# Performance work log

Hardware: AMD Instinct MI355X
Metric: run time of the kernel (lower is better)

Reference implementation:

```python
import jax, jax.numpy as jnp
import numpy as np

N = 100000
E = 1600000
IN_DIM, HID, NCLS = 256, 128, 40


def setup_inputs() -> dict:
    key = jax.random.key(0)
    ks = jax.random.split(key, 8)
    x = jax.random.normal(ks[0], (N, IN_DIM), dtype=jnp.float32)
    edge_index = jax.random.randint(ks[1], (2, E), 0, N, dtype=jnp.int32)
    def glorot(k, shape):
        lim = float(np.sqrt(6.0 / (shape[0] + shape[1])))
        return jax.random.uniform(k, shape, jnp.float32, -lim, lim)
    return {
        "x": x,
        "edge_index": edge_index,
        "W1": glorot(ks[2], (IN_DIM, HID)), "b1": jnp.zeros((HID,), jnp.float32),
        "W2": glorot(ks[3], (HID, HID)),    "b2": jnp.zeros((HID,), jnp.float32),
        "W3": glorot(ks[4], (HID, NCLS)),   "b3": jnp.zeros((NCLS,), jnp.float32),
    }


def _gcn_conv(x, src, dst, W, b):
    # dense transform first (PyG GCNConv applies lin before propagate)
    h = x @ W  # [N, out]
    # symmetric normalization with self-loops: deg over destination (in-degree)
    ones = jnp.ones(src.shape[0], dtype=x.dtype)
    deg = jax.ops.segment_sum(ones, dst, num_segments=N)
    dinv = jnp.where(deg > 0, jax.lax.rsqrt(jnp.maximum(deg, 1e-12)), 0.0)
    norm = dinv[src] * dinv[dst]  # [E+N]
    msgs = h[src] * norm[:, None]  # gather + scale
    out = jax.ops.segment_sum(msgs, dst, num_segments=N)
    return out + b


def reference(x, edge_index, W1, b1, W2, b2, W3, b3):
    # add self-loops once (same for every layer)
    loop = jnp.arange(N, dtype=edge_index.dtype)
    src = jnp.concatenate([edge_index[0], loop])
    dst = jnp.concatenate([edge_index[1], loop])
    h = _gcn_conv(x, src, dst, W1, b1)
    h = jax.nn.relu(h)  # dropout is identity in eval mode
    h = _gcn_conv(h, src, dst, W2, b2)
    h = jax.nn.relu(h)
    h = _gcn_conv(h, src, dst, W3, b3)
    return h
```

## Files before the change

### kernel.cpp

```cpp
#include <hip/hip_runtime.h>
#include <hip/hip_bf16.h>


#define WAVE 64
#define SLOTS 48
#define FILL_NR 8
#define FILL_NCHUNK 784

typedef short short8v __attribute__((ext_vector_type(8)));
typedef float f32x4 __attribute__((ext_vector_type(4)));

__device__ inline void split_bf16(float v, ushort& hi, ushort& lo) {
    __hip_bfloat16 h = __float2bfloat16(v);
    float hf = __bfloat162float(h);
    __hip_bfloat16 l = __float2bfloat16(v - hf);
    hi = *reinterpret_cast<ushort*>(&h);
    lo = *reinterpret_cast<ushort*>(&l);
}

__device__ inline float bf2f(ushort u) {
    unsigned int t = ((unsigned int)u) << 16;
    return __uint_as_float(t);
}

__device__ inline float bfLo(unsigned int u) { return __uint_as_float(u << 16); }
__device__ inline float bfHi(unsigned int u) { return __uint_as_float(u & 0xffff0000u); }

__device__ inline ushort f2bf(float v) {
    __hip_bfloat16 h = __float2bfloat16(v);
    return *reinterpret_cast<ushort*>(&h);
}


__global__ void k_fill_part(const int* __restrict__ src, const int* __restrict__ dst,
                            int* __restrict__ cnt, int* __restrict__ slots,
                            int E, int N) {
    int b = blockIdx.x;
    int r = b & (FILL_NR - 1);
    int c = b >> 3;
    int lo = (int)((long long)E * c / FILL_NCHUNK);
    int hi = (int)((long long)E * (c + 1) / FILL_NCHUNK);
    int rlo = (int)((long long)N * r / FILL_NR);
    int rhi = (int)((long long)N * (r + 1) / FILL_NR);
    for (int e = lo + threadIdx.x; e < hi; e += 256) {
        int d = dst[e];
        if (d >= rlo && d < rhi) {
            int p = atomicAdd(&cnt[d], 1);
            if (p < SLOTS) slots[(size_t)d * SLOTS + p] = src[e];
        }
    }
}

__global__ void k_dinv(const int* __restrict__ cnt, float* __restrict__ dinv, int N) {
    int i = blockIdx.x * blockDim.x + threadIdx.x;
    if (i < N) dinv[i] = rsqrtf((float)cnt[i] + 1.0f);
}


__global__ void k_wsplit(const float* __restrict__ W, ushort* __restrict__ Wth,
                         ushort* __restrict__ Wtl, int K, int M, int Mpad) {
    int idx = blockIdx.x * 256 + threadIdx.x;
    if (idx >= K * Mpad) return;
    int k = idx / Mpad, m = idx % Mpad;
    float v = (m < M) ? W[(size_t)k * M + m] : 0.f;
    ushort h, l;
    split_bf16(v, h, l);
    Wth[(size_t)m * K + k] = h;
    Wtl[(size_t)m * K + k] = l;
}


template <int K, bool BF16OUT>
__global__ __launch_bounds__(256) void gemm_mfma128(const float* __restrict__ A,
                                                    const ushort* __restrict__ Wth,
                                                    const ushort* __restrict__ Wtl,
                                                    const float* __restrict__ rowscale,
                                                    void* __restrict__ outv, int N) {
    constexpr int KC = 32;
    constexpr int LD = 40;
    __shared__ ushort Ah[128 * LD], Al[128 * LD], Bh[128 * LD], Bl[128 * LD];

    const int tid = threadIdx.x;
    const int lane = tid & 63, wave = tid >> 6;
    const int wr = (wave & 1) * 64, wc = (wave >> 1) * 64;
    const int r0 = blockIdx.x * 128;
    const int tr = lane & 15, quad = lane >> 4;

    f32x4 acc[4][4];
#pragma unroll
    for (int i = 0; i < 4; ++i)
#pragma unroll
        for (int j = 0; j < 4; ++j) acc[i][j] = (f32x4)(0.f);

    float4 pa[4];
    uint4 pbh[2], pbl[2];
    auto loadc = [&](int kc) {
#pragma unroll
        for (int u = 0; u < 4; ++u) {
            int f = tid + u * 256;
            int row = f >> 3, kq = f & 7;
            int grow = r0 + row;
            if (grow > N - 1) grow = N - 1;
            pa[u] = *reinterpret_cast<const float4*>(A + (size_t)grow * K + kc + kq * 4);
        }
#pragma unroll
        for (int u = 0; u < 2; ++u) {
            int f = tid + u * 256;
            int col = f >> 2, part = f & 3;
            pbh[u] = *reinterpret_cast<const uint4*>(Wth + (size_t)col * K + kc + part * 8);
            pbl[u] = *reinterpret_cast<const uint4*>(Wtl + (size_t)col * K + kc + part * 8);
        }
    };

    loadc(0);
    for (int kc = 0; kc < K; kc += KC) {
#pragma unroll
        for (int u = 0; u < 4; ++u) {
            int f = tid + u * 256;
            int row = f >> 3, kq = f & 7;
            float4 v = pa[u];
            ushort h0, l0, h1, l1, h2, l2, h3, l3;
            split_bf16(v.x, h0, l0);
            split_bf16(v.y, h1, l1);
            split_bf16(v.z, h2, l2);
            split_bf16(v.w, h3, l3);
            *reinterpret_cast<ushort4*>(&Ah[row * LD + kq * 4]) = make_ushort4(h0, h1, h2, h3);
            *reinterpret_cast<ushort4*>(&Al[row * LD + kq * 4]) = make_ushort4(l0, l1, l2, l3);
        }
#pragma unroll
        for (int u = 0; u < 2; ++u) {
            int f = tid + u * 256;
            int col = f >> 2, part = f & 3;
            *reinterpret_cast<uint4*>(&Bh[col * LD + part * 8]) = pbh[u];
            *reinterpret_cast<uint4*>(&Bl[col * LD + part * 8]) = pbl[u];
        }
        __syncthreads();
        if (kc + KC < K) loadc(kc + KC);
        short8v ah[4], al[4], bh[4], bl[4];
#pragma unroll
        for (int i = 0; i < 4; ++i) {
            ah[i] = *reinterpret_cast<const short8v*>(&Ah[(wr + i * 16 + tr) * LD + quad * 8]);
            al[i] = *reinterpret_cast<const short8v*>(&Al[(wr + i * 16 + tr) * LD + quad * 8]);
            bh[i] = *reinterpret_cast<const short8v*>(&Bh[(wc + i * 16 + tr) * LD + quad * 8]);
            bl[i] = *reinterpret_cast<const short8v*>(&Bl[(wc + i * 16 + tr) * LD + quad * 8]);
        }
#pragma unroll
        for (int i = 0; i < 4; ++i)
#pragma unroll
            for (int j = 0; j < 4; ++j) {
                acc[i][j] = __builtin_amdgcn_mfma_f32_16x16x32_bf16(ah[i], bh[j], acc[i][j], 0, 0, 0);
                acc[i][j] = __builtin_amdgcn_mfma_f32_16x16x32_bf16(ah[i], bl[j], acc[i][j], 0, 0, 0);
                acc[i][j] = __builtin_amdgcn_mfma_f32_16x16x32_bf16(al[i], bh[j], acc[i][j], 0, 0, 0);
            }
        __syncthreads();
    }

#pragma unroll
    for (int i = 0; i < 4; ++i) {
        int rbase = r0 + wr + i * 16 + quad * 4;
        float rs[4];
#pragma unroll
        for (int reg = 0; reg < 4; ++reg) {
            int r = rbase + reg;
            rs[reg] = (r < N) ? rowscale[r] : 0.f;
        }
#pragma unroll
        for (int j = 0; j < 4; ++j) {
            int c = wc + j * 16 + tr;
#pragma unroll
            for (int reg = 0; reg < 4; ++reg) {
                int r = rbase + reg;
                if (r < N) {
                    float v = acc[i][j][reg] * rs[reg];
                    if (BF16OUT)
                        ((ushort*)outv)[(size_t)r * 128 + c] = f2bf(v);
                    else
                        ((float*)outv)[(size_t)r * 128 + c] = v;
                }
            }
        }
    }
}


__global__ __launch_bounds__(256) void gemm_mfma40(const float* __restrict__ A,
                                                   const ushort* __restrict__ Wth,
                                                   const ushort* __restrict__ Wtl,
                                                   const float* __restrict__ rowscale,
                                                   float* __restrict__ out, int N) {
    constexpr int K = 128, KC = 32, LD = 40, M = 40;
    __shared__ ushort Ah[128 * LD], Al[128 * LD], Bh[48 * LD], Bl[48 * LD];

    const int tid = threadIdx.x;
    const int lane = tid & 63, wave = tid >> 6;
    const int wr = wave * 32;
    const int r0 = blockIdx.x * 128;
    const int tr = lane & 15, quad = lane >> 4;
    const bool hasb = tid < 192;

    f32x4 acc[2][3];
#pragma unroll
    for (int i = 0; i < 2; ++i)
#pragma unroll
        for (int j = 0; j < 3; ++j) acc[i][j] = (f32x4)(0.f);

    float4 pa[4];
    uint4 pbh0, pbl0;
    auto loadc = [&](int kc) {
#pragma unroll
        for (int u = 0; u < 4; ++u) {
            int f = tid + u * 256;
            int row = f >> 3, kq = f & 7;
            int grow = r0 + row;
            if (grow > N - 1) grow = N - 1;
            pa[u] = *reinterpret_cast<const float4*>(A + (size_t)grow * K + kc + kq * 4);
        }
        if (hasb) {
            int col = tid >> 2, part = tid & 3;
            pbh0 = *reinterpret_cast<const uint4*>(Wth + (size_t)col * K + kc + part * 8);
            pbl0 = *reinterpret_cast<const uint4*>(Wtl + (size_t)col * K + kc + part * 8);
        }
    };

    loadc(0);
    for (int kc = 0; kc < K; kc += KC) {
#pragma unroll
        for (int u = 0; u < 4; ++u) {
            int f = tid + u * 256;
            int row = f >> 3, kq = f & 7;
            float4 v = pa[u];
            ushort h0, l0, h1, l1, h2, l2, h3, l3;
            split_bf16(v.x, h0, l0);
            split_bf16(v.y, h1, l1);
            split_bf16(v.z, h2, l2);
            split_bf16(v.w, h3, l3);
            *reinterpret_cast<ushort4*>(&Ah[row * LD + kq * 4]) = make_ushort4(h0, h1, h2, h3);
            *reinterpret_cast<ushort4*>(&Al[row * LD + kq * 4]) = make_ushort4(l0, l1, l2, l3);
        }
        if (hasb) {
            int col = tid >> 2, part = tid & 3;
            *reinterpret_cast<uint4*>(&Bh[col * LD + part * 8]) = pbh0;
            *reinterpret_cast<uint4*>(&Bl[col * LD + part * 8]) = pbl0;
        }
        __syncthreads();
        if (kc + KC < K) loadc(kc + KC);
        short8v ah[2], al[2], bh[3], bl[3];
#pragma unroll
        for (int i = 0; i < 2; ++i) {
            ah[i] = *reinterpret_cast<const short8v*>(&Ah[(wr + i * 16 + tr) * LD + quad * 8]);
            al[i] = *reinterpret_cast<const short8v*>(&Al[(wr + i * 16 + tr) * LD + quad * 8]);
        }
#pragma unroll
        for (int j = 0; j < 3; ++j) {
            bh[j] = *reinterpret_cast<const short8v*>(&Bh[(j * 16 + tr) * LD + quad * 8]);
            bl[j] = *reinterpret_cast<const short8v*>(&Bl[(j * 16 + tr) * LD + quad * 8]);
        }
#pragma unroll
        for (int i = 0; i < 2; ++i)
#pragma unroll
            for (int j = 0; j < 3; ++j) {
                acc[i][j] = __builtin_amdgcn_mfma_f32_16x16x32_bf16(ah[i], bh[j], acc[i][j], 0, 0, 0);
                acc[i][j] = __builtin_amdgcn_mfma_f32_16x16x32_bf16(ah[i], bl[j], acc[i][j], 0, 0, 0);
                acc[i][j] = __builtin_amdgcn_mfma_f32_16x16x32_bf16(al[i], bh[j], acc[i][j], 0, 0, 0);
            }
        __syncthreads();
    }

#pragma unroll
    for (int i = 0; i < 2; ++i) {
        int rbase = r0 + wr + i * 16 + quad * 4;
        float rs[4];
#pragma unroll
        for (int reg = 0; reg < 4; ++reg) {
            int r = rbase + reg;
            rs[reg] = (r < N) ? rowscale[r] : 0.f;
        }
#pragma unroll
        for (int j = 0; j < 3; ++j) {
            int c = j * 16 + tr;
#pragma unroll
            for (int reg = 0; reg < 4; ++reg) {
                int r = rbase + reg;
                if (r < N && c < M) out[(size_t)r * M + c] = acc[i][j][reg] * rs[reg];
            }
        }
    }
}


template <bool RELU>
__global__ __launch_bounds__(256) void agg128_bf4(const ushort* __restrict__ S,
                                                  const int* __restrict__ slots,
                                                  const int* __restrict__ cnt,
                                                  const float* __restrict__ dinv,
                                                  const float* __restrict__ bias,
                                                  float* __restrict__ out, int N) {
    int w = (blockIdx.x * blockDim.x + threadIdx.x) >> 6;
    int lane = threadIdx.x & 63;
    int nquad = (N + 3) >> 2;
    if (w >= nquad) return;
    int part = lane >> 4, sub = lane & 15;
    int node = 4 * w + part;
    bool valid = node < N;
    int snode = valid ? node : 0;
    const uint4* S8 = (const uint4*)S;
    const int* row = slots + (size_t)snode * SLOTS;
    int c = valid ? cnt[snode] : 0;
    if (c > SLOTS) c = SLOTS;
    int cm = max(c, __shfl(c, lane ^ 16));
    cm = max(cm, __shfl(cm, lane ^ 32));

    uint4 sv = S8[(size_t)snode * 16 + sub];
    float a0 = bfLo(sv.x), a1 = bfHi(sv.x), a2 = bfLo(sv.y), a3 = bfHi(sv.y);
    float a4 = bfLo(sv.z), a5 = bfHi(sv.z), a6 = bfLo(sv.w), a7 = bfHi(sv.w);

    int e = 0;
    for (; e + 8 <= cm; e += 8) {
        int s[8];
#pragma unroll
        for (int u = 0; u < 8; ++u) s[u] = (e + u < c) ? row[e + u] : snode;
        uint4 v[8];
#pragma unroll
        for (int u = 0; u < 8; ++u) v[u] = S8[(size_t)s[u] * 16 + sub];
#pragma unroll
        for (int u = 0; u < 8; ++u) {
            float m = (e + u < c) ? 1.f : 0.f;
            a0 += m * bfLo(v[u].x);
            a1 += m * bfHi(v[u].x);
            a2 += m * bfLo(v[u].y);
            a3 += m * bfHi(v[u].y);
            a4 += m * bfLo(v[u].z);
            a5 += m * bfHi(v[u].z);
            a6 += m * bfLo(v[u].w);
            a7 += m * bfHi(v[u].w);
        }
    }
    for (; e < cm; ++e) {
        int s = (e < c) ? row[e] : snode;
        uint4 v = S8[(size_t)s * 16 + sub];
        float m = (e < c) ? 1.f : 0.f;
        a0 += m * bfLo(v.x);
        a1 += m * bfHi(v.x);
        a2 += m * bfLo(v.y);
        a3 += m * bfHi(v.y);
        a4 += m * bfLo(v.z);
        a5 += m * bfHi(v.z);
        a6 += m * bfLo(v.w);
        a7 += m * bfHi(v.w);
    }

    if (valid) {
        float di = dinv[node];
        float4 b0 = ((const float4*)bias)[sub * 2];
        float4 b1 = ((const float4*)bias)[sub * 2 + 1];
        float o0 = a0 * di + b0.x, o1 = a1 * di + b0.y, o2 = a2 * di + b0.z, o3 = a3 * di + b0.w;
        float o4 = a4 * di + b1.x, o5 = a5 * di + b1.y, o6 = a6 * di + b1.z, o7 = a7 * di + b1.w;
        if (RELU) {
            o0 = fmaxf(o0, 0.f); o1 = fmaxf(o1, 0.f); o2 = fmaxf(o2, 0.f); o3 = fmaxf(o3, 0.f);
            o4 = fmaxf(o4, 0.f); o5 = fmaxf(o5, 0.f); o6 = fmaxf(o6, 0.f); o7 = fmaxf(o7, 0.f);
        }
        ((float4*)out)[(size_t)node * 32 + sub * 2] = make_float4(o0, o1, o2, o3);
        ((float4*)out)[(size_t)node * 32 + sub * 2 + 1] = make_float4(o4, o5, o6, o7);
    }
}

__global__ __launch_bounds__(256) void agg40(const float* __restrict__ S,
                                             const int* __restrict__ slots,
                                             const int* __restrict__ cnt,
                                             const float* __restrict__ dinv,
                                             const float* __restrict__ bias,
                                             float* __restrict__ out, int N) {
    int wid = (blockIdx.x * blockDim.x + threadIdx.x) >> 6;
    int lane = threadIdx.x & 63;
    if (wid >= N || lane >= 40) return;
    const int* row = slots + (size_t)wid * SLOTS;
    int c = cnt[wid];
    if (c > SLOTS) c = SLOTS;
    float acc = S[(size_t)wid * 40 + lane];
    int e = 0;
    for (; e + 8 <= c; e += 8) {
        int s[8];
#pragma unroll
        for (int u = 0; u < 8; ++u) s[u] = row[e + u];
        float v[8];
#pragma unroll
        for (int u = 0; u < 8; ++u) v[u] = S[(size_t)s[u] * 40 + lane];
#pragma unroll
        for (int u = 0; u < 8; ++u) acc += v[u];
    }
    for (; e < c; ++e) acc += S[(size_t)row[e] * 40 + lane];
    out[(size_t)wid * 40 + lane] = acc * dinv[wid] + bias[lane];
}


extern "C" void kernel_launch(void* const* d_in, const int* in_sizes, int n_in,
                              void* d_out, int out_size, void* d_ws, size_t ws_size,
                              hipStream_t stream) {
    const float* x  = (const float*)d_in[0];
    const int*   ei = (const int*)d_in[1];
    const float* W1 = (const float*)d_in[2];
    const float* b1 = (const float*)d_in[3];
    const float* W2 = (const float*)d_in[4];
    const float* b2 = (const float*)d_in[5];
    const float* W3 = (const float*)d_in[6];
    const float* b3 = (const float*)d_in[7];
    float* out = (float*)d_out;

    const int IN_DIM = 256, HID = 128;
    const int N = in_sizes[0] / IN_DIM;
    const int E = in_sizes[1] / 2;
    const int* srcE = ei;
    const int* dstE = ei + E;

    char* ws = (char*)d_ws;
    size_t off = 0;
    auto alloc = [&](size_t bytes) -> void* {
        off = (off + 255) & ~(size_t)255;
        void* p = ws + off;
        off += bytes;
        return p;
    };
    int*    cnt   = (int*)alloc((size_t)N * 4);
    float*  dinv  = (float*)alloc((size_t)N * 4);
    int*    slots = (int*)alloc((size_t)N * SLOTS * 4);
    ushort* bufS  = (ushort*)alloc((size_t)N * HID * 4);
    float*  bufH  = (float*)alloc((size_t)N * HID * 4);
    ushort* W1th  = (ushort*)alloc((size_t)128 * 256 * 2);
    ushort* W1tl  = (ushort*)alloc((size_t)128 * 256 * 2);
    ushort* W2th  = (ushort*)alloc((size_t)128 * 128 * 2);
    ushort* W2tl  = (ushort*)alloc((size_t)128 * 128 * 2);
    ushort* W3th  = (ushort*)alloc((size_t)48 * 128 * 2);
    ushort* W3tl  = (ushort*)alloc((size_t)48 * 128 * 2);

    const int NB = (N + 255) / 256;
    const int AGGB = (N * WAVE + 255) / 256;
    const int AGG4B = (((N + 3) / 4) * WAVE + 255) / 256;
    const int GB = (N + 127) / 128;
    const int FB = FILL_NR * FILL_NCHUNK;

    k_wsplit<<<(256 * 128 + 255) / 256, 256, 0, stream>>>(W1, W1th, W1tl, 256, 128, 128);
    k_wsplit<<<(128 * 128 + 255) / 256, 256, 0, stream>>>(W2, W2th, W2tl, 128, 128, 128);
    k_wsplit<<<(128 * 48 + 255) / 256, 256, 0, stream>>>(W3, W3th, W3tl, 128, 40, 48);

    hipMemsetAsync(cnt, 0, (size_t)N * 4, stream);
    k_fill_part<<<FB, 256, 0, stream>>>(srcE, dstE, cnt, slots, E, N);
    k_dinv<<<NB, 256, 0, stream>>>(cnt, dinv, N);

    gemm_mfma128<256, true><<<GB, 256, 0, stream>>>(x, W1th, W1tl, dinv, bufS, N);
    agg128_bf4<true><<<AGG4B, 256, 0, stream>>>(bufS, slots, cnt, dinv, b1, bufH, N);
    gemm_mfma128<128, true><<<GB, 256, 0, stream>>>(bufH, W2th, W2tl, dinv, bufS, N);
    agg128_bf4<true><<<AGG4B, 256, 0, stream>>>(bufS, slots, cnt, dinv, b2, bufH, N);
    gemm_mfma40<<<GB, 256, 0, stream>>>(bufH, W3th, W3tl, dinv, (float*)bufS, N);
    agg40<<<AGGB, 256, 0, stream>>>((float*)bufS, slots, cnt, dinv, b3, out, N);
}
```

Before: 592.1 us.

## Replace LDS-staged GEMMs with per-wave register-direct MFMA tiles

```diff
diff --git a/kernel.cpp b/kernel.cpp
--- a/kernel.cpp
+++ b/kernel.cpp
@@ -18,17 +18,23 @@
     lo = *reinterpret_cast<ushort*>(&l);
 }
 
-__device__ inline float bf2f(ushort u) {
-    unsigned int t = ((unsigned int)u) << 16;
-    return __uint_as_float(t);
-}
-
 __device__ inline float bfLo(unsigned int u) { return __uint_as_float(u << 16); }
 __device__ inline float bfHi(unsigned int u) { return __uint_as_float(u & 0xffff0000u); }
 
 __device__ inline ushort f2bf(float v) {
     __hip_bfloat16 h = __float2bfloat16(v);
     return *reinterpret_cast<ushort*>(&h);
+}
+
+__device__ inline void split8(float4 v0, float4 v1, short8v& h, short8v& l) {
+    float f[8] = {v0.x, v0.y, v0.z, v0.w, v1.x, v1.y, v1.z, v1.w};
+#pragma unroll
+    for (int i = 0; i < 8; ++i) {
+        ushort hh, ll;
+        split_bf16(f[i], hh, ll);
+        h[i] = (short)hh;
+        l[i] = (short)ll;
+    }
 }
 
 
@@ -71,19 +77,16 @@
 
 
 template <int K, bool BF16OUT>
-__global__ __launch_bounds__(256) void gemm_mfma128(const float* __restrict__ A,
-                                                    const ushort* __restrict__ Wth,
-                                                    const ushort* __restrict__ Wtl,
-                                                    const float* __restrict__ rowscale,
-                                                    void* __restrict__ outv, int N) {
-    constexpr int KC = 32;
-    constexpr int LD = 40;
-    __shared__ ushort Ah[128 * LD], Al[128 * LD], Bh[128 * LD], Bl[128 * LD];
-
-    const int tid = threadIdx.x;
-    const int lane = tid & 63, wave = tid >> 6;
-    const int wr = (wave & 1) * 64, wc = (wave >> 1) * 64;
-    const int r0 = blockIdx.x * 128;
+__global__ __launch_bounds__(256) void gemm_nolds128(const float* __restrict__ A,
+                                                     const ushort* __restrict__ Wth,
+                                                     const ushort* __restrict__ Wtl,
+                                                     const float* __restrict__ rowscale,
+                                                     void* __restrict__ outv, int N) {
+    const int wave = threadIdx.x >> 6, lane = threadIdx.x & 63;
+    const int nstrips = (N + 63) >> 6;
+    const int job = blockIdx.x * 4 + wave;
+    if (job >= nstrips * 2) return;
+    const int r0 = (job >> 1) * 64, c0 = (job & 1) * 64;
     const int tr = lane & 15, quad = lane >> 4;
 
     f32x4 acc[4][4];
@@ -92,57 +95,22 @@
 #pragma unroll
         for (int j = 0; j < 4; ++j) acc[i][j] = (f32x4)(0.f);
 
-    float4 pa[4];
-    uint4 pbh[2], pbl[2];
-    auto loadc = [&](int kc) {
-#pragma unroll
-        for (int u = 0; u < 4; ++u) {
-            int f = tid + u * 256;
-            int row = f >> 3, kq = f & 7;
-            int grow = r0 + row;
-            if (grow > N - 1) grow = N - 1;
-            pa[u] = *reinterpret_cast<const float4*>(A + (size_t)grow * K + kc + kq * 4);
-        }
-#pragma unroll
-        for (int u = 0; u < 2; ++u) {
-            int f = tid + u * 256;
-            int col = f >> 2, part = f & 3;
-            pbh[u] = *reinterpret_cast<const uint4*>(Wth + (size_t)col * K + kc + part * 8);
-            pbl[u] = *reinterpret_cast<const uint4*>(Wtl + (size_t)col * K + kc + part * 8);
-        }
-    };
-
-    loadc(0);
-    for (int kc = 0; kc < K; kc += KC) {
-#pragma unroll
-        for (int u = 0; u < 4; ++u) {
-            int f = tid + u * 256;
-            int row = f >> 3, kq = f & 7;
-            float4 v = pa[u];
-            ushort h0, l0, h1, l1, h2, l2, h3, l3;
-            split_bf16(v.x, h0, l0);
-            split_bf16(v.y, h1, l1);
-            split_bf16(v.z, h2, l2);
-            split_bf16(v.w, h3, l3);
-            *reinterpret_cast<ushort4*>(&Ah[row * LD + kq * 4]) = make_ushort4(h0, h1, h2, h3);
-            *reinterpret_cast<ushort4*>(&Al[row * LD + kq * 4]) = make_ushort4(l0, l1, l2, l3);
-        }
-#pragma unroll
-        for (int u = 0; u < 2; ++u) {
-            int f = tid + u * 256;
-            int col = f >> 2, part = f & 3;
-            *reinterpret_cast<uint4*>(&Bh[col * LD + part * 8]) = pbh[u];
-            *reinterpret_cast<uint4*>(&Bl[col * LD + part * 8]) = pbl[u];
-        }
-        __syncthreads();
-        if (kc + KC < K) loadc(kc + KC);
+    for (int kc = 0; kc < K; kc += 32) {
         short8v ah[4], al[4], bh[4], bl[4];
 #pragma unroll
         for (int i = 0; i < 4; ++i) {
-            ah[i] = *reinterpret_cast<const short8v*>(&Ah[(wr + i * 16 + tr) * LD + quad * 8]);
-            al[i] = *reinterpret_cast<const short8v*>(&Al[(wr + i * 16 + tr) * LD + quad * 8]);
-            bh[i] = *reinterpret_cast<const short8v*>(&Bh[(wc + i * 16 + tr) * LD + quad * 8]);
-            bl[i] = *reinterpret_cast<const short8v*>(&Bl[(wc + i * 16 + tr) * LD + quad * 8]);
+            int r = r0 + i * 16 + tr;
+            if (r > N - 1) r = N - 1;
+            const float* p = A + (size_t)r * K + kc + quad * 8;
+            float4 v0 = *reinterpret_cast<const float4*>(p);
+            float4 v1 = *reinterpret_cast<const float4*>(p + 4);
+            split8(v0, v1, ah[i], al[i]);
+        }
+#pragma unroll
+        for (int j = 0; j < 4; ++j) {
+            int c = c0 + j * 16 + tr;
+            bh[j] = *reinterpret_cast<const short8v*>(Wth + (size_t)c * K + kc + quad * 8);
+            bl[j] = *reinterpret_cast<const short8v*>(Wtl + (size_t)c * K + kc + quad * 8);
         }
 #pragma unroll
         for (int i = 0; i < 4; ++i)
@@ -152,12 +120,11 @@
                 acc[i][j] = __builtin_amdgcn_mfma_f32_16x16x32_bf16(ah[i], bl[j], acc[i][j], 0, 0, 0);
                 acc[i][j] = __builtin_amdgcn_mfma_f32_16x16x32_bf16(al[i], bh[j], acc[i][j], 0, 0, 0);
             }
-        __syncthreads();
     }
 
 #pragma unroll
     for (int i = 0; i < 4; ++i) {
-        int rbase = r0 + wr + i * 16 + quad * 4;
+        int rbase = r0 + i * 16 + quad * 4;
         float rs[4];
 #pragma unroll
         for (int reg = 0; reg < 4; ++reg) {
@@ -166,7 +133,7 @@
         }
 #pragma unroll
         for (int j = 0; j < 4; ++j) {
-            int c = wc + j * 16 + tr;
+            int c = c0 + j * 16 + tr;
 #pragma unroll
             for (int reg = 0; reg < 4; ++reg) {
                 int r = rbase + reg;
@@ -183,92 +150,55 @@
 }
 
 
-__global__ __launch_bounds__(256) void gemm_mfma40(const float* __restrict__ A,
-                                                   const ushort* __restrict__ Wth,
-                                                   const ushort* __restrict__ Wtl,
-                                                   const float* __restrict__ rowscale,
-                                                   float* __restrict__ out, int N) {
-    constexpr int K = 128, KC = 32, LD = 40, M = 40;
-    __shared__ ushort Ah[128 * LD], Al[128 * LD], Bh[48 * LD], Bl[48 * LD];
-
-    const int tid = threadIdx.x;
-    const int lane = tid & 63, wave = tid >> 6;
-    const int wr = wave * 32;
-    const int r0 = blockIdx.x * 128;
+__global__ __launch_bounds__(256) void gemm_nolds40(const float* __restrict__ A,
+                                                    const ushort* __restrict__ Wth,
+                                                    const ushort* __restrict__ Wtl,
+                                                    const float* __restrict__ rowscale,
+                                                    float* __restrict__ out, int N) {
+    constexpr int K = 128, M = 40;
+    const int wave = threadIdx.x >> 6, lane = threadIdx.x & 63;
+    const int nstrips = (N + 63) >> 6;
+    const int job = blockIdx.x * 4 + wave;
+    if (job >= nstrips) return;
+    const int r0 = job * 64;
     const int tr = lane & 15, quad = lane >> 4;
-    const bool hasb = tid < 192;
-
-    f32x4 acc[2][3];
-#pragma unroll
-    for (int i = 0; i < 2; ++i)
+
+    f32x4 acc[4][3];
+#pragma unroll
+    for (int i = 0; i < 4; ++i)
 #pragma unroll
         for (int j = 0; j < 3; ++j) acc[i][j] = (f32x4)(0.f);
 
-    float4 pa[4];
-    uint4 pbh0, pbl0;
-    auto loadc = [&](int kc) {
-#pragma unroll
-        for (int u = 0; u < 4; ++u) {
-            int f = tid + u * 256;
-            int row = f >> 3, kq = f & 7;
-            int grow = r0 + row;
-            if (grow > N - 1) grow = N - 1;
-            pa[u] = *reinterpret_cast<const float4*>(A + (size_t)grow * K + kc + kq * 4);
-        }
-        if (hasb) {
-            int col = tid >> 2, part = tid & 3;
-            pbh0 = *reinterpret_cast<const uint4*>(Wth + (size_t)col * K + kc + part * 8);
-            pbl0 = *reinterpret_cast<const uint4*>(Wtl + (size_t)col * K + kc + part * 8);
-        }
-    };
-
-    loadc(0);
-    for (int kc = 0; kc < K; kc += KC) {
-#pragma unroll
-        for (int u = 0; u < 4; ++u) {
-            int f = tid + u * 256;
-            int row = f >> 3, kq = f & 7;
-            float4 v = pa[u];
-            ushort h0, l0, h1, l1, h2, l2, h3, l3;
-            split_bf16(v.x, h0, l0);
-            split_bf16(v.y, h1, l1);
-            split_bf16(v.z, h2, l2);
-            split_bf16(v.w, h3, l3);
-            *reinterpret_cast<ushort4*>(&Ah[row * LD + kq * 4]) = make_ushort4(h0, h1, h2, h3);
-            *reinterpret_cast<ushort4*>(&Al[row * LD + kq * 4]) = make_ushort4(l0, l1, l2, l3);
-        }
-        if (hasb) {
-            int col = tid >> 2, part = tid & 3;
-            *reinterpret_cast<uint4*>(&Bh[col * LD + part * 8]) = pbh0;
-            *reinterpret_cast<uint4*>(&Bl[col * LD + part * 8]) = pbl0;
-        }
-        __syncthreads();
-        if (kc + KC < K) loadc(kc + KC);
-        short8v ah[2], al[2], bh[3], bl[3];
-#pragma unroll
-        for (int i = 0; i < 2; ++i) {
-            ah[i] = *reinterpret_cast<const short8v*>(&Ah[(wr + i * 16 + tr) * LD + quad * 8]);
-            al[i] = *reinterpret_cast<const short8v*>(&Al[(wr + i * 16 + tr) * LD + quad * 8]);
+    for (int kc = 0; kc < K; kc += 32) {
+        short8v ah[4], al[4], bh[3], bl[3];
+#pragma unroll
+        for (int i = 0; i < 4; ++i) {
+            int r = r0 + i * 16 + tr;
+            if (r > N - 1) r = N - 1;
+            const float* p = A + (size_t)r * K + kc + quad * 8;
+            float4 v0 = *reinterpret_cast<const float4*>(p);
+            float4 v1 = *reinterpret_cast<const float4*>(p + 4);
+            split8(v0, v1, ah[i], al[i]);
         }
 #pragma unroll
         for (int j = 0; j < 3; ++j) {
-            bh[j] = *reinterpret_cast<const short8v*>(&Bh[(j * 16 + tr) * LD + quad * 8]);
-            bl[j] = *reinterpret_cast<const short8v*>(&Bl[(j * 16 + tr) * LD + quad * 8]);
-        }
-#pragma unroll
-        for (int i = 0; i < 2; ++i)
+            int c = j * 16 + tr;
+            bh[j] = *reinterpret_cast<const short8v*>(Wth + (size_t)c * K + kc + quad * 8);
+            bl[j] = *reinterpret_cast<const short8v*>(Wtl + (size_t)c * K + kc + quad * 8);
+        }
+#pragma unroll
+        for (int i = 0; i < 4; ++i)
 #pragma unroll
             for (int j = 0; j < 3; ++j) {
                 acc[i][j] = __builtin_amdgcn_mfma_f32_16x16x32_bf16(ah[i], bh[j], acc[i][j], 0, 0, 0);
                 acc[i][j] = __builtin_amdgcn_mfma_f32_16x16x32_bf16(ah[i], bl[j], acc[i][j], 0, 0, 0);
                 acc[i][j] = __builtin_amdgcn_mfma_f32_16x16x32_bf16(al[i], bh[j], acc[i][j], 0, 0, 0);
             }
-        __syncthreads();
-    }
-
-#pragma unroll
-    for (int i = 0; i < 2; ++i) {
-        int rbase = r0 + wr + i * 16 + quad * 4;
+    }
+
+#pragma unroll
+    for (int i = 0; i < 4; ++i) {
+        int rbase = r0 + i * 16 + quad * 4;
         float rs[4];
 #pragma unroll
         for (int reg = 0; reg < 4; ++reg) {
@@ -435,8 +365,10 @@
     const int NB = (N + 255) / 256;
     const int AGGB = (N * WAVE + 255) / 256;
     const int AGG4B = (((N + 3) / 4) * WAVE + 255) / 256;
-    const int GB = (N + 127) / 128;
     const int FB = FILL_NR * FILL_NCHUNK;
+    const int nstrips = (N + 63) / 64;
+    const int GB128 = (nstrips * 2 + 3) / 4;
+    const int GB40 = (nstrips + 3) / 4;
 
     k_wsplit<<<(256 * 128 + 255) / 256, 256, 0, stream>>>(W1, W1th, W1tl, 256, 128, 128);
     k_wsplit<<<(128 * 128 + 255) / 256, 256, 0, stream>>>(W2, W2th, W2tl, 128, 128, 128);
@@ -446,10 +378,10 @@
     k_fill_part<<<FB, 256, 0, stream>>>(srcE, dstE, cnt, slots, E, N);
     k_dinv<<<NB, 256, 0, stream>>>(cnt, dinv, N);
 
-    gemm_mfma128<256, true><<<GB, 256, 0, stream>>>(x, W1th, W1tl, dinv, bufS, N);
+    gemm_nolds128<256, true><<<GB128, 256, 0, stream>>>(x, W1th, W1tl, dinv, bufS, N);
     agg128_bf4<true><<<AGG4B, 256, 0, stream>>>(bufS, slots, cnt, dinv, b1, bufH, N);
-    gemm_mfma128<128, true><<<GB, 256, 0, stream>>>(bufH, W2th, W2tl, dinv, bufS, N);
+    gemm_nolds128<128, true><<<GB128, 256, 0, stream>>>(bufH, W2th, W2tl, dinv, bufS, N);
     agg128_bf4<true><<<AGG4B, 256, 0, stream>>>(bufS, slots, cnt, dinv, b2, bufH, N);
-    gemm_mfma40<<<GB, 256, 0, stream>>>(bufH, W3th, W3tl, dinv, (float*)bufS, N);
+    gemm_nolds40<<<GB40, 256, 0, stream>>>(bufH, W3th, W3tl, dinv, (float*)bufS, N);
     agg40<<<AGGB, 256, 0, stream>>>((float*)bufS, slots, cnt, dinv, b3, out, N);
 }
```

After: 597.5 us. About the same (+0.9%).
